# Performance work log

Measured on AMD Instinct MI355X. Metric: run time of the kernel, lower is better.

Reference implementation:

```python
import jax, jax.numpy as jnp
import numpy as np

EPS = 1e-6  # eps assumed for rms/unit norm (repo uses a small eps; math identical up to eps)

def rms_norm(x):
    # normalize so RMS over last dim == 1
    return x * jax.lax.rsqrt(jnp.mean(x * x, axis=-1, keepdims=True) + EPS)

def unit_norm(w):
    # normalize each output row of the weight to unit L2 norm
    return w * jax.lax.rsqrt(jnp.sum(w * w, axis=-1, keepdims=True) + EPS)

def setup_inputs() -> dict:
    key = jax.random.key(0)
    k1, k2, k3 = jax.random.split(key, 3)
    B, S, D = 4, 2048, 2048
    x = jax.random.normal(k1, (B, S, D), dtype=jnp.float32)
    w_in = jax.random.normal(k2, (3 * D, D), dtype=jnp.float32)
    w_out = jax.random.normal(k3, (D, D), dtype=jnp.float32)
    return {"x": x, "w_in": w_in, "w_out": w_out}

def reference(x, w_in, w_out):
    B, S, D = x.shape
    H = 16
    hd = D // H
    # MPLinear in-projection with unit-normalized weight rows
    qkv = jnp.einsum("bsd,fd->bsf", x, unit_norm(w_in))  # [B,S,3D]
    qkv = qkv.reshape(B, S, 3, H, hd).transpose(2, 0, 3, 1, 4)  # [3,B,H,S,hd]
    q, k, v = qkv[0], qkv[1], qkv[2]
    q = rms_norm(q)
    k = rms_norm(k)
    # scaled dot product attention, causal, default scale 1/sqrt(hd)
    scores = jnp.einsum("bhqd,bhkd->bhqk", q, k) / jnp.sqrt(jnp.float32(hd))
    causal_mask = jnp.tril(jnp.ones((S, S), dtype=bool))
    scores = jnp.where(causal_mask, scores, jnp.finfo(scores.dtype).min)
    attn = jax.nn.softmax(scores, axis=-1)
    a = jnp.einsum("bhqk,bhkd->bhqd", attn, v)  # [B,H,S,hd]
    a = rms_norm(a)
    a = a.transpose(0, 2, 1, 3).reshape(B, S, D)
    return jnp.einsum("bsd,fd->bsf", a, unit_norm(w_out))
```

## Files before the change

kernel.cpp:

```cpp
#include <hip/hip_runtime.h>

typedef float f32x4 __attribute__((ext_vector_type(4)));
typedef __bf16 bf16x8 __attribute__((ext_vector_type(8)));

#define EPSF 1e-6f
#define AS1 __attribute__((address_space(1)))
#define AS3 __attribute__((address_space(3)))

__device__ static inline void gl_lds16(const __bf16* g, __bf16* l) {
  __builtin_amdgcn_global_load_lds((const AS1 void*)g, (AS3 void*)l, 16, 0, 0);
}

__global__ __launch_bounds__(256) void norm_w(const float* __restrict__ w_in,
                                              const float* __restrict__ w_out,
                                              __bf16* __restrict__ w_in_n,
                                              __bf16* __restrict__ w_out_n) {
  __shared__ float red[4];
  const int row = blockIdx.x;
  const float* src = (row < 6144) ? (w_in + (size_t)row * 2048)
                                  : (w_out + (size_t)(row - 6144) * 2048);
  __bf16* dst = (row < 6144) ? (w_in_n + (size_t)row * 2048)
                             : (w_out_n + (size_t)(row - 6144) * 2048);
  const int t = threadIdx.x;
  float4 v[2];
  float ss = 0.f;
#pragma unroll
  for (int i = 0; i < 2; i++) {
    v[i] = ((const float4*)src)[t + i * 256];
    ss += v[i].x * v[i].x + v[i].y * v[i].y + v[i].z * v[i].z + v[i].w * v[i].w;
  }
#pragma unroll
  for (int m = 32; m >= 1; m >>= 1) ss += __shfl_xor(ss, m);
  if ((t & 63) == 0) red[t >> 6] = ss;
  __syncthreads();
  float tot = red[0] + red[1] + red[2] + red[3];
  float sc = rsqrtf(tot + EPSF);
#pragma unroll
  for (int i = 0; i < 2; i++) {
    int c0 = (t + i * 256) * 4;
    dst[c0 + 0] = (__bf16)(v[i].x * sc);
    dst[c0 + 1] = (__bf16)(v[i].y * sc);
    dst[c0 + 2] = (__bf16)(v[i].z * sc);
    dst[c0 + 3] = (__bf16)(v[i].w * sc);
  }
}

__global__ __launch_bounds__(256) void cast_x(const float* __restrict__ x,
                                              __bf16* __restrict__ xb) {
  size_t i = ((size_t)blockIdx.x * 256 + threadIdx.x) * 8;
  float4 a = ((const float4*)(x + i))[0];
  float4 b = ((const float4*)(x + i))[1];
  bf16x8 o;
  o[0] = (__bf16)a.x; o[1] = (__bf16)a.y; o[2] = (__bf16)a.z; o[3] = (__bf16)a.w;
  o[4] = (__bf16)b.x; o[5] = (__bf16)b.y; o[6] = (__bf16)b.z; o[7] = (__bf16)b.w;
  *(bf16x8*)(xb + i) = o;
}

#define LDSOFF(r_, blk_) ((r_) * 64 + (((blk_) ^ ((r_) & 7)) * 8))
#define SA(bb_, c_, kt_) gl_lds16(gA + (long)(c_) * 64 * K + (long)(kt_) * 64, &As[bb_][(c_) * 4096 + t * 8])
#define SB(bb_, c_, kt_) gl_lds16(gB + (long)(c_) * 64 * K + (long)(kt_) * 64, &Bs[bb_][(c_) * 4096 + t * 8])

template <int MODE>
__global__ __launch_bounds__(512) void gemm8(const __bf16* __restrict__ A,
                                             const __bf16* __restrict__ W,
                                             float* __restrict__ C,
                                             __bf16* __restrict__ Cb,
                                             __bf16* __restrict__ Vtb,
                                             int M, int N, int K) {
  __shared__ __bf16 As[2][16384];
  __shared__ __bf16 Bs[2][16384];
  __shared__ float rsum[8][128];

  const int gx = gridDim.x;
  const int nwg = gx * gridDim.y;
  int wg = blockIdx.y * gx + blockIdx.x;
  wg = (wg & 7) * (nwg >> 3) + (wg >> 3);
  const int bx = wg % gx, by = wg / gx;

  const int t = threadIdx.x;
  const int lane = t & 63, w = t >> 6;
  const int wr = w >> 2, wc = w & 3;
  const int wrb = wr * 128, wcb = wc * 64;
  const int fr = lane & 15, fq = lane >> 4;
  const long m0 = (long)by * 256;
  const long n0 = (long)bx * 256;
  const int NT = K >> 6;

  const int srow = t >> 3;
  const int sblk = (t & 7) ^ (srow & 7);
  const __bf16* gA = A + (m0 + srow) * (long)K + sblk * 8;
  const __bf16* gB = W + (n0 + srow) * (long)K + sblk * 8;

  f32x4 acc[8][4];
#pragma unroll
  for (int i = 0; i < 8; i++)
#pragma unroll
    for (int j = 0; j < 4; j++)
#pragma unroll
      for (int c = 0; c < 4; c++) acc[i][j][c] = 0.f;

  bf16x8 a0[4][2], a1[4][2], b01[2][2], b23[2][2];

  SA(0, 0, 0); SA(0, 2, 0);
  SB(0, 0, 0); SB(0, 1, 0);
  SB(0, 2, 0); SB(0, 3, 0);
  SA(0, 1, 0); SA(0, 3, 0);
  SA(1, 0, 1); SA(1, 2, 1);
  SB(1, 0, 1); SB(1, 1, 1);
  SB(1, 2, 1); SB(1, 3, 1);
  asm volatile("s_waitcnt vmcnt(6)" ::: "memory");
  __builtin_amdgcn_s_barrier();

  auto tile_step = [&](int kt, int b) {
#pragma unroll
    for (int i = 0; i < 4; i++)
#pragma unroll
      for (int ks = 0; ks < 2; ks++)
        a0[i][ks] = *(const bf16x8*)&As[b][LDSOFF(wrb + i * 16 + fr, ks * 4 + fq)];
#pragma unroll
    for (int j = 0; j < 2; j++)
#pragma unroll
      for (int ks = 0; ks < 2; ks++)
        b01[j][ks] = *(const bf16x8*)&Bs[b][LDSOFF(wcb + j * 16 + fr, ks * 4 + fq)];
    if (kt + 1 < NT) { SA(b ^ 1, 1, kt + 1); SA(b ^ 1, 3, kt + 1); }
    __builtin_amdgcn_s_barrier();
    asm volatile("s_waitcnt lgkmcnt(0)" ::: "memory");
    __builtin_amdgcn_sched_barrier(0);
    __builtin_amdgcn_s_setprio(1);
#pragma unroll
    for (int i = 0; i < 4; i++)
#pragma unroll
      for (int j = 0; j < 2; j++)
#pragma unroll
        for (int ks = 0; ks < 2; ks++)
          acc[i][j] = __builtin_amdgcn_mfma_f32_16x16x32_bf16(a0[i][ks], b01[j][ks], acc[i][j], 0, 0, 0);
    __builtin_amdgcn_s_setprio(0);
    __builtin_amdgcn_s_barrier();

#pragma unroll
    for (int j = 0; j < 2; j++)
#pragma unroll
      for (int ks = 0; ks < 2; ks++)
        b23[j][ks] = *(const bf16x8*)&Bs[b][LDSOFF(wcb + (2 + j) * 16 + fr, ks * 4 + fq)];
    if (kt + 2 < NT) { SA(b, 0, kt + 2); SA(b, 2, kt + 2); }
    __builtin_amdgcn_s_barrier();
    asm volatile("s_waitcnt lgkmcnt(0)" ::: "memory");
    __builtin_amdgcn_sched_barrier(0);
    __builtin_amdgcn_s_setprio(1);
#pragma unroll
    for (int i = 0; i < 4; i++)
#pragma unroll
      for (int j = 0; j < 2; j++)
#pragma unroll
        for (int ks = 0; ks < 2; ks++)
          acc[i][2 + j] = __builtin_amdgcn_mfma_f32_16x16x32_bf16(a0[i][ks], b23[j][ks], acc[i][2 + j], 0, 0, 0);
    __builtin_amdgcn_s_setprio(0);
    __builtin_amdgcn_s_barrier();

#pragma unroll
    for (int i = 0; i < 4; i++)
#pragma unroll
      for (int ks = 0; ks < 2; ks++)
        a1[i][ks] = *(const bf16x8*)&As[b][LDSOFF(wrb + 64 + i * 16 + fr, ks * 4 + fq)];
    if (kt + 2 < NT) { SB(b, 0, kt + 2); SB(b, 1, kt + 2); }
    __builtin_amdgcn_s_barrier();
    asm volatile("s_waitcnt lgkmcnt(0)" ::: "memory");
    __builtin_amdgcn_sched_barrier(0);
    __builtin_amdgcn_s_setprio(1);
#pragma unroll
    for (int i = 0; i < 4; i++)
#pragma unroll
      for (int j = 0; j < 2; j++)
#pragma unroll
        for (int ks = 0; ks < 2; ks++)
          acc[4 + i][j] = __builtin_amdgcn_mfma_f32_16x16x32_bf16(a1[i][ks], b01[j][ks], acc[4 + i][j], 0, 0, 0);
    __builtin_amdgcn_s_setprio(0);
    __builtin_amdgcn_s_barrier();

    if (kt + 2 < NT) { SB(b, 2, kt + 2); SB(b, 3, kt + 2); }
    __builtin_amdgcn_s_setprio(1);
#pragma unroll
    for (int i = 0; i < 4; i++)
#pragma unroll
      for (int j = 0; j < 2; j++)
#pragma unroll
        for (int ks = 0; ks < 2; ks++)
          acc[4 + i][2 + j] = __builtin_amdgcn_mfma_f32_16x16x32_bf16(a1[i][ks], b23[j][ks], acc[4 + i][2 + j], 0, 0, 0);
    __builtin_amdgcn_s_setprio(0);
    if (kt >= NT - 2)
      asm volatile("s_waitcnt vmcnt(0)" ::: "memory");
    else
      asm volatile("s_waitcnt vmcnt(6)" ::: "memory");
    __builtin_amdgcn_s_barrier();
  };

  for (int kt = 0; kt < NT; kt += 2) {
    tile_step(kt, 0);
    tile_step(kt + 1, 1);
  }

  if (MODE == 0) {
#pragma unroll
    for (int i = 0; i < 8; i++)
#pragma unroll
      for (int j = 0; j < 4; j++)
#pragma unroll
        for (int r = 0; r < 4; r++) {
          long row = m0 + wrb + i * 16 + fq * 4 + r;
          long col = n0 + wcb + j * 16 + fr;
          C[row * N + col] = acc[i][j][r];
        }
  } else {
    const int tt = (int)(n0 >> 11);
    const int hh = (int)(((n0 >> 7) + (wc >> 1)) & 15);
    const long e0 = (long)(wc & 1) * 64;
    if (tt < 2) {
#pragma unroll
      for (int i = 0; i < 8; i++)
#pragma unroll
        for (int r = 0; r < 4; r++) {
          float s2 = 0.f;
#pragma unroll
          for (int j = 0; j < 4; j++) s2 += acc[i][j][r] * acc[i][j][r];
          s2 += __shfl_xor(s2, 1);
          s2 += __shfl_xor(s2, 2);
          s2 += __shfl_xor(s2, 4);
          s2 += __shfl_xor(s2, 8);
          if (fr == 0) rsum[w][i * 16 + fq * 4 + r] = s2;
        }
      __syncthreads();
#pragma unroll
      for (int i = 0; i < 8; i++)
#pragma unroll
        for (int r = 0; r < 4; r++) {
          int rl = i * 16 + fq * 4 + r;
          float tot = rsum[w][rl] + rsum[w ^ 1][rl];
          float sc = rsqrtf(tot * (1.f / 128.f) + EPSF);
          long row = m0 + wrb + rl;
          long bb = row >> 11, ss = row & 2047;
          __bf16* base = Cb + ((((long)tt * 4 + bb) * 16 + hh) * 2048 + ss) * 128 + e0;
#pragma unroll
          for (int j = 0; j < 4; j++)
            base[j * 16 + fr] = (__bf16)(acc[i][j][r] * sc);
        }
    } else {
#pragma unroll
      for (int i = 0; i < 8; i++)
#pragma unroll
        for (int r = 0; r < 4; r++) {
          long row = m0 + wrb + i * 16 + fq * 4 + r;
          long bb = row >> 11, ss = row & 2047;
#pragma unroll
          for (int j = 0; j < 4; j++)
            Vtb[((bb * 16 + hh) * 128 + e0 + j * 16 + fr) * 2048 + ss] = (__bf16)acc[i][j][r];
        }
    }
  }
}

__global__ __launch_bounds__(512) void attn(const __bf16* __restrict__ qkv,
                                            const __bf16* __restrict__ vt,
                                            __bf16* __restrict__ an) {
  __shared__ __bf16 Ks[64 * 128];
  __shared__ __bf16 Vs[128 * 64];
  __shared__ __bf16 plds[8][16 * 40];
  const int L = blockIdx.x;
  const int qt = L >> 6;
  const int bh = (L & 7) + 8 * ((L >> 3) & 7);
  const int t = threadIdx.x;
  const int lane = t & 63, w = t >> 6;
  const int fr = lane & 15, fq = lane >> 4;
  const int swz = fr & 7;
  const __bf16* Q = qkv + (long)bh * 262144;
  const __bf16* Kbh = qkv + 16777216L + (long)bh * 262144;
  const __bf16* Vbh = vt + (long)bh * 262144;
  __bf16* pw = plds[w];
  const float sc2 = 0.08838834764831845f * 1.4426950408889634f;
  const float MFIX = 20.0f;
  const int b = bh >> 4, h = bh & 15;

  const __bf16* gK = Kbh + (long)(t >> 4) * 128 + ((t & 15) ^ ((t >> 4) & 7)) * 8;
  const __bf16* gV = Vbh + (long)(t >> 3) * 2048 + ((t & 7) ^ ((t >> 3) & 7)) * 8;
  __bf16* lK = &Ks[t * 8];
  __bf16* lV = &Vs[t * 8];

#pragma unroll 1
  for (int side = 0; side < 2; side++) {
    const int qi = side ? (15 - qt) : qt;
    const int q0 = qi * 128 + w * 16;
    const int cha = q0 >> 5;
    bf16x8 qf[4];
#pragma unroll
    for (int ec = 0; ec < 4; ec++)
      qf[ec] = *(const bf16x8*)(Q + (long)(q0 + fr) * 128 + ec * 32 + fq * 8);
    float lacc[4];
#pragma unroll
    for (int r = 0; r < 4; r++) lacc[r] = 0.f;
    f32x4 oacc[8];
#pragma unroll
    for (int e = 0; e < 8; e++)
#pragma unroll
      for (int c = 0; c < 4; c++) oacc[e][c] = 0.f;

    const int nst = 2 * qi + 2;
#pragma unroll 1
    for (int st = 0; st < nst; st++) {
      const int k0 = st * 64;
      gl_lds16(gK + (long)k0 * 128, lK);
      gl_lds16(gK + (long)(k0 + 32) * 128, lK + 4096);
      gl_lds16(gV + k0, lV);
      gl_lds16(gV + 64L * 2048 + k0, lV + 4096);
      __syncthreads();
#pragma unroll
      for (int half = 0; half < 2; half++) {
        const int k32 = k0 + half * 32;
        const int ch = k32 >> 5;
        if (ch <= cha) {
          f32x4 sa[2];
#pragma unroll
          for (int ct = 0; ct < 2; ct++)
#pragma unroll
            for (int c = 0; c < 4; c++) sa[ct][c] = 0.f;
#pragma unroll
          for (int ct = 0; ct < 2; ct++) {
#pragma unroll
            for (int ec = 0; ec < 4; ec++) {
              bf16x8 kf = *(const bf16x8*)(&Ks[(half * 32 + ct * 16 + fr) * 128 +
                                               ((ec * 4 + fq) ^ swz) * 8]);
              sa[ct] = __builtin_amdgcn_mfma_f32_16x16x32_bf16(qf[ec], kf, sa[ct], 0, 0, 0);
            }
          }
          if (ch == cha) {
#pragma unroll
            for (int r = 0; r < 4; r++) {
              int qg = q0 + fq * 4 + r;
              float p0 = exp2f(((k32 + fr) <= qg) ? sa[0][r] * sc2 - MFIX : -1e30f);
              float p1 = exp2f(((k32 + 16 + fr) <= qg) ? sa[1][r] * sc2 - MFIX : -1e30f);
              lacc[r] += p0 + p1;
              pw[(fq * 4 + r) * 40 + fr] = (__bf16)p0;
              pw[(fq * 4 + r) * 40 + 16 + fr] = (__bf16)p1;
            }
          } else {
#pragma unroll
            for (int r = 0; r < 4; r++) {
              float p0 = exp2f(__builtin_fmaf(sa[0][r], sc2, -MFIX));
              float p1 = exp2f(__builtin_fmaf(sa[1][r], sc2, -MFIX));
              lacc[r] += p0 + p1;
              pw[(fq * 4 + r) * 40 + fr] = (__bf16)p0;
              pw[(fq * 4 + r) * 40 + 16 + fr] = (__bf16)p1;
            }
          }
          bf16x8 pa = *(const bf16x8*)(&pw[fr * 40 + fq * 8]);
#pragma unroll
          for (int e = 0; e < 8; e++) {
            bf16x8 vf = *(const bf16x8*)(&Vs[(e * 16 + fr) * 64 +
                                             ((half * 4 + fq) ^ swz) * 8]);
            oacc[e] = __builtin_amdgcn_mfma_f32_16x16x32_bf16(pa, vf, oacc[e], 0, 0, 0);
          }
        }
      }
      __syncthreads();
    }
#pragma unroll
    for (int r = 0; r < 4; r++) {
      float ls = lacc[r];
      ls += __shfl_xor(ls, 1);
      ls += __shfl_xor(ls, 2);
      ls += __shfl_xor(ls, 4);
      ls += __shfl_xor(ls, 8);
      float inv = 1.0f / ls;
      float ssq = 0.f;
#pragma unroll
      for (int e = 0; e < 8; e++) { float v = oacc[e][r] * inv; ssq += v * v; }
      ssq += __shfl_xor(ssq, 1);
      ssq += __shfl_xor(ssq, 2);
      ssq += __shfl_xor(ssq, 4);
      ssq += __shfl_xor(ssq, 8);
      float rsc = rsqrtf(ssq * (1.f / 128.f) + EPSF) * inv;
      long s = q0 + fq * 4 + r;
      __bf16* dst = an + ((long)b * 2048 + s) * 2048 + h * 128;
#pragma unroll
      for (int e = 0; e < 8; e++) dst[e * 16 + fr] = (__bf16)(oacc[e][r] * rsc);
    }
  }
}

extern "C" void kernel_launch(void* const* d_in, const int* in_sizes, int n_in,
                              void* d_out, int out_size, void* d_ws, size_t ws_size,
                              hipStream_t stream) {
  const float* x = (const float*)d_in[0];
  const float* w_in = (const float*)d_in[1];
  const float* w_out = (const float*)d_in[2];
  float* out = (float*)d_out;
  char* ws = (char*)d_ws;

  __bf16* w_in_n = (__bf16*)(ws);
  __bf16* w_out_n = (__bf16*)(ws + 25165824);
  __bf16* xb = (__bf16*)(ws + 33554432);
  __bf16* an = xb;
  __bf16* qkv = (__bf16*)(ws + 67108864);
  __bf16* vt = (__bf16*)(ws + 167772160);

  norm_w<<<8192, 256, 0, stream>>>(w_in, w_out, w_in_n, w_out_n);
  cast_x<<<8192, 256, 0, stream>>>(x, xb);
  gemm8<1><<<dim3(24, 32), 512, 0, stream>>>(xb, w_in_n, nullptr, qkv, vt, 8192, 6144, 2048);
  attn<<<512, 512, 0, stream>>>(qkv, vt, an);
  gemm8<0><<<dim3(8, 32), 512, 0, stream>>>(an, w_out_n, out, nullptr, nullptr, 8192, 2048, 2048);
}
```

Measured before the change: 510.9 us.

## Merge weight-norm and x-cast kernels; trim GEMM barriers and reorder prefetch issue

Combines the weight normalization and x-to-bf16 cast into one launch, indexed by block ID, so one kernel launch and its gap go away. In the GEMM main loop it removes the pre-MFMA s_barrier/lgkmcnt waits and sched_barriers and places sched_barriers after the MFMA groups. It also merges the B-prefetch issues into one point and scopes the fragment registers per phase. This cuts synchronization overhead in the GEMM, at the risk that compiler-inserted waits serialize differently and that register pressure or LDS read ordering changes.

```diff
diff --git a/kernel.cpp b/kernel.cpp
--- a/kernel.cpp
+++ b/kernel.cpp
@@ -11,49 +11,50 @@
   __builtin_amdgcn_global_load_lds((const AS1 void*)g, (AS3 void*)l, 16, 0, 0);
 }
 
-__global__ __launch_bounds__(256) void norm_w(const float* __restrict__ w_in,
-                                              const float* __restrict__ w_out,
-                                              __bf16* __restrict__ w_in_n,
-                                              __bf16* __restrict__ w_out_n) {
+__global__ __launch_bounds__(256) void prep(const float* __restrict__ x,
+                                            const float* __restrict__ w_in,
+                                            const float* __restrict__ w_out,
+                                            __bf16* __restrict__ xb,
+                                            __bf16* __restrict__ w_in_n,
+                                            __bf16* __restrict__ w_out_n) {
   __shared__ float red[4];
-  const int row = blockIdx.x;
-  const float* src = (row < 6144) ? (w_in + (size_t)row * 2048)
-                                  : (w_out + (size_t)(row - 6144) * 2048);
-  __bf16* dst = (row < 6144) ? (w_in_n + (size_t)row * 2048)
-                             : (w_out_n + (size_t)(row - 6144) * 2048);
+  const int bid = blockIdx.x;
   const int t = threadIdx.x;
-  float4 v[2];
-  float ss = 0.f;
-#pragma unroll
-  for (int i = 0; i < 2; i++) {
-    v[i] = ((const float4*)src)[t + i * 256];
-    ss += v[i].x * v[i].x + v[i].y * v[i].y + v[i].z * v[i].z + v[i].w * v[i].w;
+  if (bid < 8192) {
+    const float* src = (bid < 6144) ? (w_in + (size_t)bid * 2048)
+                                    : (w_out + (size_t)(bid - 6144) * 2048);
+    __bf16* dst = (bid < 6144) ? (w_in_n + (size_t)bid * 2048)
+                               : (w_out_n + (size_t)(bid - 6144) * 2048);
+    float4 v[2];
+    float ss = 0.f;
+#pragma unroll
+    for (int i = 0; i < 2; i++) {
+      v[i] = ((const float4*)src)[t + i * 256];
+      ss += v[i].x * v[i].x + v[i].y * v[i].y + v[i].z * v[i].z + v[i].w * v[i].w;
+    }
+#pragma unroll
+    for (int m = 32; m >= 1; m >>= 1) ss += __shfl_xor(ss, m);
+    if ((t & 63) == 0) red[t >> 6] = ss;
+    __syncthreads();
+    float tot = red[0] + red[1] + red[2] + red[3];
+    float sc = rsqrtf(tot + EPSF);
+#pragma unroll
+    for (int i = 0; i < 2; i++) {
+      int c0 = (t + i * 256) * 4;
+      dst[c0 + 0] = (__bf16)(v[i].x * sc);
+      dst[c0 + 1] = (__bf16)(v[i].y * sc);
+      dst[c0 + 2] = (__bf16)(v[i].z * sc);
+      dst[c0 + 3] = (__bf16)(v[i].w * sc);
+    }
+  } else {
+    size_t i = ((size_t)(bid - 8192) * 256 + t) * 8;
+    float4 a = ((const float4*)(x + i))[0];
+    float4 b = ((const float4*)(x + i))[1];
+    bf16x8 o;
+    o[0] = (__bf16)a.x; o[1] = (__bf16)a.y; o[2] = (__bf16)a.z; o[3] = (__bf16)a.w;
+    o[4] = (__bf16)b.x; o[5] = (__bf16)b.y; o[6] = (__bf16)b.z; o[7] = (__bf16)b.w;
+    *(bf16x8*)(xb + i) = o;
   }
-#pragma unroll
-  for (int m = 32; m >= 1; m >>= 1) ss += __shfl_xor(ss, m);
-  if ((t & 63) == 0) red[t >> 6] = ss;
-  __syncthreads();
-  float tot = red[0] + red[1] + red[2] + red[3];
-  float sc = rsqrtf(tot + EPSF);
-#pragma unroll
-  for (int i = 0; i < 2; i++) {
-    int c0 = (t + i * 256) * 4;
-    dst[c0 + 0] = (__bf16)(v[i].x * sc);
-    dst[c0 + 1] = (__bf16)(v[i].y * sc);
-    dst[c0 + 2] = (__bf16)(v[i].z * sc);
-    dst[c0 + 3] = (__bf16)(v[i].w * sc);
-  }
-}
-
-__global__ __launch_bounds__(256) void cast_x(const float* __restrict__ x,
-                                              __bf16* __restrict__ xb) {
-  size_t i = ((size_t)blockIdx.x * 256 + threadIdx.x) * 8;
-  float4 a = ((const float4*)(x + i))[0];
-  float4 b = ((const float4*)(x + i))[1];
-  bf16x8 o;
-  o[0] = (__bf16)a.x; o[1] = (__bf16)a.y; o[2] = (__bf16)a.z; o[3] = (__bf16)a.w;
-  o[4] = (__bf16)b.x; o[5] = (__bf16)b.y; o[6] = (__bf16)b.z; o[7] = (__bf16)b.w;
-  *(bf16x8*)(xb + i) = o;
 }
 
 #define LDSOFF(r_, blk_) ((r_) * 64 + (((blk_) ^ ((r_) & 7)) * 8))
@@ -99,19 +100,15 @@
 #pragma unroll
       for (int c = 0; c < 4; c++) acc[i][j][c] = 0.f;
 
-  bf16x8 a0[4][2], a1[4][2], b01[2][2], b23[2][2];
-
-  SA(0, 0, 0); SA(0, 2, 0);
-  SB(0, 0, 0); SB(0, 1, 0);
-  SB(0, 2, 0); SB(0, 3, 0);
-  SA(0, 1, 0); SA(0, 3, 0);
+  SA(0, 0, 0); SA(0, 1, 0); SA(0, 2, 0); SA(0, 3, 0);
+  SB(0, 0, 0); SB(0, 1, 0); SB(0, 2, 0); SB(0, 3, 0);
   SA(1, 0, 1); SA(1, 2, 1);
-  SB(1, 0, 1); SB(1, 1, 1);
-  SB(1, 2, 1); SB(1, 3, 1);
+  SB(1, 0, 1); SB(1, 1, 1); SB(1, 2, 1); SB(1, 3, 1);
   asm volatile("s_waitcnt vmcnt(6)" ::: "memory");
   __builtin_amdgcn_s_barrier();
 
   auto tile_step = [&](int kt, int b) {
+    bf16x8 a0[4][2], b01[2][2];
 #pragma unroll
     for (int i = 0; i < 4; i++)
 #pragma unroll
@@ -123,9 +120,6 @@
       for (int ks = 0; ks < 2; ks++)
         b01[j][ks] = *(const bf16x8*)&Bs[b][LDSOFF(wcb + j * 16 + fr, ks * 4 + fq)];
     if (kt + 1 < NT) { SA(b ^ 1, 1, kt + 1); SA(b ^ 1, 3, kt + 1); }
-    __builtin_amdgcn_s_barrier();
-    asm volatile("s_waitcnt lgkmcnt(0)" ::: "memory");
-    __builtin_amdgcn_sched_barrier(0);
     __builtin_amdgcn_s_setprio(1);
 #pragma unroll
     for (int i = 0; i < 4; i++)
@@ -135,17 +129,16 @@
         for (int ks = 0; ks < 2; ks++)
           acc[i][j] = __builtin_amdgcn_mfma_f32_16x16x32_bf16(a0[i][ks], b01[j][ks], acc[i][j], 0, 0, 0);
     __builtin_amdgcn_s_setprio(0);
+    __builtin_amdgcn_sched_barrier(0);
     __builtin_amdgcn_s_barrier();
 
+    bf16x8 b23[2][2];
 #pragma unroll
     for (int j = 0; j < 2; j++)
 #pragma unroll
       for (int ks = 0; ks < 2; ks++)
         b23[j][ks] = *(const bf16x8*)&Bs[b][LDSOFF(wcb + (2 + j) * 16 + fr, ks * 4 + fq)];
     if (kt + 2 < NT) { SA(b, 0, kt + 2); SA(b, 2, kt + 2); }
-    __builtin_amdgcn_s_barrier();
-    asm volatile("s_waitcnt lgkmcnt(0)" ::: "memory");
-    __builtin_amdgcn_sched_barrier(0);
     __builtin_amdgcn_s_setprio(1);
 #pragma unroll
     for (int i = 0; i < 4; i++)
@@ -155,17 +148,16 @@
         for (int ks = 0; ks < 2; ks++)
           acc[i][2 + j] = __builtin_amdgcn_mfma_f32_16x16x32_bf16(a0[i][ks], b23[j][ks], acc[i][2 + j], 0, 0, 0);
     __builtin_amdgcn_s_setprio(0);
+    __builtin_amdgcn_sched_barrier(0);
     __builtin_amdgcn_s_barrier();
 
+    bf16x8 a1[4][2];
 #pragma unroll
     for (int i = 0; i < 4; i++)
 #pragma unroll
       for (int ks = 0; ks < 2; ks++)
         a1[i][ks] = *(const bf16x8*)&As[b][LDSOFF(wrb + 64 + i * 16 + fr, ks * 4 + fq)];
-    if (kt + 2 < NT) { SB(b, 0, kt + 2); SB(b, 1, kt + 2); }
-    __builtin_amdgcn_s_barrier();
-    asm volatile("s_waitcnt lgkmcnt(0)" ::: "memory");
-    __builtin_amdgcn_sched_barrier(0);
+    if (kt + 2 < NT) { SB(b, 0, kt + 2); SB(b, 1, kt + 2); SB(b, 2, kt + 2); SB(b, 3, kt + 2); }
     __builtin_amdgcn_s_setprio(1);
 #pragma unroll
     for (int i = 0; i < 4; i++)
@@ -174,11 +166,6 @@
 #pragma unroll
         for (int ks = 0; ks < 2; ks++)
           acc[4 + i][j] = __builtin_amdgcn_mfma_f32_16x16x32_bf16(a1[i][ks], b01[j][ks], acc[4 + i][j], 0, 0, 0);
-    __builtin_amdgcn_s_setprio(0);
-    __builtin_amdgcn_s_barrier();
-
-    if (kt + 2 < NT) { SB(b, 2, kt + 2); SB(b, 3, kt + 2); }
-    __builtin_amdgcn_s_setprio(1);
 #pragma unroll
     for (int i = 0; i < 4; i++)
 #pragma unroll
@@ -191,6 +178,7 @@
       asm volatile("s_waitcnt vmcnt(0)" ::: "memory");
     else
       asm volatile("s_waitcnt vmcnt(6)" ::: "memory");
+    __builtin_amdgcn_sched_barrier(0);
     __builtin_amdgcn_s_barrier();
   };
 
@@ -401,8 +389,7 @@
   __bf16* qkv = (__bf16*)(ws + 67108864);
   __bf16* vt = (__bf16*)(ws + 167772160);
 
-  norm_w<<<8192, 256, 0, stream>>>(w_in, w_out, w_in_n, w_out_n);
-  cast_x<<<8192, 256, 0, stream>>>(x, xb);
+  prep<<<16384, 256, 0, stream>>>(x, w_in, w_out, xb, w_in_n, w_out_n);
   gemm8<1><<<dim3(24, 32), 512, 0, stream>>>(xb, w_in_n, nullptr, qkv, vt, 8192, 6144, 2048);
   attn<<<512, 512, 0, stream>>>(qkv, vt, an);
   gemm8<0><<<dim3(8, 32), 512, 0, stream>>>(an, w_out_n, out, nullptr, nullptr, 8192, 2048, 2048);
```

Result: no change. 513.9 us (+0.6%).
